# Performance work log

Measured on AMD Instinct MI355X. Metric: run time of the kernel, lower is better.

## Reference

```python
import jax, jax.numpy as jnp
import numpy as np

B, S, NH = 8, 32, 8
N = S * S + 1            # 1 extra (cls) token + S*S image tokens
C = 512
D = C // NH
SCALE = D ** -0.5
LAM = 0.6


def _ln(x, w, b, eps=1e-5):
    m = x.mean(-1, keepdims=True)
    v = ((x - m) ** 2).mean(-1, keepdims=True)
    return (x - m) / jnp.sqrt(v + eps) * w + b


def _rel_index():
    ch, cw = np.meshgrid(np.arange(S), np.arange(S), indexing='ij')
    cf = np.stack([ch.ravel(), cw.ravel()])            # [2, S*S]
    rel = (cf[:, :, None] - cf[:, None, :]).transpose(1, 2, 0).astype(np.int64)
    rel[..., 0] += S - 1
    rel[..., 1] += S - 1
    rel[..., 0] *= 2 * S - 1
    idx = rel.sum(-1)                                  # [n, n]
    out = np.zeros((N, N), dtype=np.int64)             # F.pad with 0 for extra token row/col
    out[1:, 1:] = idx
    return jnp.asarray(out)


def setup_inputs():
    key = jax.random.key(0)
    ks = jax.random.split(key, 8)
    std = 0.02
    return {
        'x': jax.random.normal(ks[0], (B, N, C), jnp.float32),
        'ln1_w': jnp.ones((C,), jnp.float32), 'ln1_b': jnp.zeros((C,), jnp.float32),
        'qkv_w': jax.random.normal(ks[1], (3 * C, C), jnp.float32) * std,
        'rpb_table': jax.random.normal(ks[2], ((2 * S - 1) * (2 * S - 1) + 1, NH), jnp.float32) * std,
        'proj_w': jax.random.normal(ks[3], (C, C), jnp.float32) * std,
        'proj_b': jnp.zeros((C,), jnp.float32),
        'token_weights': jnp.array([0.5, 0.5], jnp.float32),
        'ln2_w': jnp.ones((C,), jnp.float32), 'ln2_b': jnp.zeros((C,), jnp.float32),
        'fc1_w': jax.random.normal(ks[4], (4 * C, C), jnp.float32) * std,
        'fc1_b': jnp.zeros((4 * C,), jnp.float32),
        'fc2_w': jax.random.normal(ks[5], (C, 4 * C), jnp.float32) * std,
        'fc2_b': jnp.zeros((C,), jnp.float32),
        'rel_index': _rel_index(),
        'H': S, 'W': S,
    }


def _attn_core(xn, qkv_w, rpb_table, rel_index):
    qkv = (xn @ qkv_w.T).reshape(B, N, 3, NH, D).transpose(2, 0, 3, 1, 4)
    q, k, v = qkv[0] * SCALE, qkv[1], qkv[2]           # [B, NH, N, D]
    bias = rpb_table[rel_index].transpose(2, 0, 1)     # [NH, N, N] bias-table gather
    attn = jax.nn.softmax(jnp.einsum('bhnd,bhmd->bhnm', q, k) + bias[None], axis=-1)
    out = jnp.einsum('bhnm,bhmd->bhnd', attn, v).transpose(0, 2, 1, 3).reshape(B, N, C)
    return attn, out


def _plan(attn, token_weights):
    # Non-differentiable token-selection plan (pure index computation).
    a = np.asarray(attn)
    cls = a[:, :, 0, 1:].mean(axis=1)                  # [B, n] head-averaged cls->image attn
    n = cls.shape[1]
    avg = cls.mean(1, keepdims=True)
    mx = cls.max(1, keepdims=True)
    counts = ((cls >= avg) & (cls <= mx)).sum(1)
    max_value = int(counts.max())
    T = float(counts.mean())
    sig = 1.0 / (1.0 + np.exp(-(max_value - T) / B))
    keep = int(round(n * (LAM + (1.0 - LAM) * sig)))
    top = np.argsort(-cls, axis=1)[:, :keep].reshape(-1)   # per-batch top-k, flattened
    _, first = np.unique(top, return_index=True)
    sel = top[np.sort(first)][:keep]                   # dedup (first occurrence), truncate
    remaining = N - (1 + keep)
    w = np.asarray(jax.nn.softmax(token_weights))
    nt = int(w[0] * remaining)
    ni = remaining - nt
    kk = jax.random.key(1234)
    ti = jax.random.randint(kk, (B, nt), 0, 1)         # text pool has exactly 1 token
    ii = jax.random.randint(jax.random.fold_in(kk, 1), (B, ni), 0, n - 1)
    return jnp.asarray(sel), ti, ii


def _gather_tok(t, idx):
    return jnp.take_along_axis(t, jnp.broadcast_to(idx[:, :, None], idx.shape + (t.shape[-1],)), axis=1)


def _assemble(xo, xn, sel, ti, ii):
    parts = [xo[:, :1], xo[:, 1:][:, sel],             # kept extra + selected image tokens
             _gather_tok(xn[:, 1:2], ti),              # random 'text' filler from y=xn
             _gather_tok(xn[:, 2:], ii)]               # random 'image' filler from y=xn
    return jnp.concatenate(parts, axis=1)


def reference(x, ln1_w, ln1_b, qkv_w, rpb_table, proj_w, proj_b, token_weights, ln2_w, ln2_b, fc1_w, fc1_b, fc2_w, fc2_b, rel_index, H, W):
    xn = _ln(x, ln1_w, ln1_b)
    attn, out = _attn_core(xn, qkv_w, rpb_table, rel_index)
    xo = out @ proj_w.T + proj_b
    sel, ti, ii = _plan(attn, token_weights)
    x1 = x + _assemble(xo, xn, sel, ti, ii)
    h = _ln(x1, ln2_w, ln2_b)
    h = jax.nn.gelu(h @ fc1_w.T + fc1_b, approximate=False)
    return x1 + (h @ fc2_w.T + fc2_b)
```

## Files before the change

### kernel.cpp

```cpp
#include <hip/hip_runtime.h>
#include <cmath>

#define PARTITIONABLE 1

constexpr int B_ = 8;
constexpr int N_ = 1025;
constexpr int C_ = 512;
constexpr int NH_ = 8;
constexpr int D_ = 64;
constexpr int K3_ = 1536;
constexpr int F_ = 2048;
constexpr int ROWS_ = B_ * N_;
constexpr int NXCD_ = 8;
constexpr int WCONV_BLKS_ = (K3_ * C_ + C_ * C_ + F_ * C_ + C_ * F_) / 1024;

constexpr size_t BYTE_XN      = 0;
constexpr size_t BYTE_QKVBF   = 16793600;
constexpr size_t BYTE_XNBF    = 41984000;
constexpr size_t BYTE_HBUF    = 16793600;
constexpr size_t BYTE_WTAIL   = 60882944;
constexpr size_t BYTE_ATTNBF  = 67174400;
constexpr size_t BYTE_X1NBF   = 75571200;
constexpr size_t BYTE_XO      = 83968000;
constexpr size_t BYTE_X1      = 100761600;
constexpr size_t PLAN_BYTE    = 117555200;

typedef unsigned short u16;
typedef __attribute__((ext_vector_type(4))) unsigned short u16x4;
typedef __attribute__((ext_vector_type(8))) short bf16x8;
typedef __attribute__((ext_vector_type(4))) float f32x4;

__device__ inline u16 f2bf(float f) {
  unsigned u = __float_as_uint(f);
  u = (u + 0x7FFFu + ((u >> 16) & 1u)) >> 16;
  return (u16)u;
}
__device__ inline float bf2f(u16 u) { return __uint_as_float(((unsigned)u) << 16); }

__device__ inline int xcd_swz(int bid, int nwg) {
  const int xcd = bid % NXCD_, i = bid / NXCD_;
  const int q = nwg / NXCD_, r = nwg % NXCD_;
  const int base = (xcd < r) ? xcd * (q + 1) : r * (q + 1) + (xcd - r) * q;
  return base + i;
}

__device__ inline void gload_lds16(const void* g, void* l) {
  __builtin_amdgcn_global_load_lds(
      (const __attribute__((address_space(1))) void*)g,
      (__attribute__((address_space(3))) void*)l, 16, 0, 0);
}

__global__ __launch_bounds__(256) void ln_wconv_kernel(
    const float* __restrict__ x, const float* __restrict__ w,
    const float* __restrict__ b, float* __restrict__ of, u16* __restrict__ ob,
    const float* __restrict__ w0, const float* __restrict__ w1,
    const float* __restrict__ w2, const float* __restrict__ w3,
    u16* __restrict__ o0, u16* __restrict__ o1,
    u16* __restrict__ o2, u16* __restrict__ o3) {
  __shared__ float red[4];
  if (blockIdx.x >= ROWS_) {
    constexpr int n0 = K3_ * C_, n1 = C_ * C_, n2 = F_ * C_;
    const int idx4 = ((blockIdx.x - ROWS_) * 256 + threadIdx.x) * 4;
    const float* src;
    u16* dst;
    int off;
    if (idx4 < n0) { src = w0; dst = o0; off = idx4; }
    else if (idx4 < n0 + n1) { src = w1; dst = o1; off = idx4 - n0; }
    else if (idx4 < n0 + n1 + n2) { src = w2; dst = o2; off = idx4 - n0 - n1; }
    else { src = w3; dst = o3; off = idx4 - n0 - n1 - n2; }
    const float4 v = *(const float4*)(src + off);
    u16x4 r;
    r.x = f2bf(v.x); r.y = f2bf(v.y); r.z = f2bf(v.z); r.w = f2bf(v.w);
    *(u16x4*)(dst + off) = r;
    return;
  }
  const int r = blockIdx.x;
  const int t = threadIdx.x;
  const float* xr = x + (size_t)r * C_;
  float v0 = xr[t], v1 = xr[t + 256];
  float s = v0 + v1;
#pragma unroll
  for (int o = 32; o; o >>= 1) s += __shfl_down(s, o);
  if ((t & 63) == 0) red[t >> 6] = s;
  __syncthreads();
  const float mean = (red[0] + red[1] + red[2] + red[3]) * (1.0f / 512.0f);
  __syncthreads();
  const float d0 = v0 - mean, d1 = v1 - mean;
  float q = d0 * d0 + d1 * d1;
#pragma unroll
  for (int o = 32; o; o >>= 1) q += __shfl_down(q, o);
  if ((t & 63) == 0) red[t >> 6] = q;
  __syncthreads();
  const float var = (red[0] + red[1] + red[2] + red[3]) * (1.0f / 512.0f);
  const float inv = 1.0f / sqrtf(var + 1e-5f);
  const float r0 = d0 * inv * w[t] + b[t];
  const float r1 = d1 * inv * w[t + 256] + b[t + 256];
  of[(size_t)r * C_ + t] = r0;
  of[(size_t)r * C_ + t + 256] = r1;
  ob[(size_t)r * C_ + t] = f2bf(r0);
  ob[(size_t)r * C_ + t + 256] = f2bf(r1);
}

template <int BN, int ACT, bool RES, bool OUTBF, bool QSCALE>
__global__ __launch_bounds__(256) void gemm_bf_kernel(
    const u16* __restrict__ A, const u16* __restrict__ W,
    const float* __restrict__ bias, const float* __restrict__ resid,
    void* __restrict__ outp, int M, int K, int Nout) {
  constexpr int WN = BN / 2;
  constexpr int NJ = WN / 16;
  constexpr int BPW = (BN / 8) / 4;
  __shared__ alignas(16) u16 As[2][128][64];
  __shared__ alignas(16) u16 Bs[2][BN][64];
  const int tid = threadIdx.x;
  const int ny = Nout / BN;
  const int l = xcd_swz(blockIdx.x, gridDim.x);
  const int m0 = (l / ny) * 128, n0 = (l % ny) * BN;
  const int wave = tid >> 6, lane = tid & 63;
  const int wr = wave >> 1, wc = wave & 1;
  const int lrow = lane & 15, lgrp = lane >> 4;
  const int srow = lane >> 3;
  const int soff = (16 * (lane & 7)) ^ (16 * srow);
  const int nk = K >> 6;

  auto stage = [&](int k0, int bufi) {
#pragma unroll
    for (int c = 0; c < 4; ++c) {
      const int q = wave * 4 + c;
      const int row = q * 8 + srow;
      int gm = m0 + row;
      if (gm >= M) gm = M - 1;
      gload_lds16((const char*)(A + (size_t)gm * K + k0) + soff,
                  (char*)&As[bufi][0][0] + (q << 10));
    }
#pragma unroll
    for (int c = 0; c < BPW; ++c) {
      const int q = wave * BPW + c;
      const int row = q * 8 + srow;
      gload_lds16((const char*)(W + (size_t)(n0 + row) * K + k0) + soff,
                  (char*)&Bs[bufi][0][0] + (q << 10));
    }
  };

  f32x4 acc[4][NJ] = {};
  stage(0, 0);
  int buf = 0;
  for (int t = 0; t < nk; ++t) {
    if (t + 1 < nk) {
      stage((t + 1) << 6, buf ^ 1);
      if constexpr (BN == 128) asm volatile("s_waitcnt vmcnt(8)" ::: "memory");
      else                     asm volatile("s_waitcnt vmcnt(6)" ::: "memory");
    } else {
      asm volatile("s_waitcnt vmcnt(0)" ::: "memory");
    }
    __builtin_amdgcn_sched_barrier(0);
    __builtin_amdgcn_s_barrier();
    const char* asb = (const char*)&As[buf][0][0];
    const char* bsb = (const char*)&Bs[buf][0][0];
    __builtin_amdgcn_s_setprio(1);
#pragma unroll
    for (int ch = 0; ch < 2; ++ch) {
      bf16x8 af[4], bfv[NJ];
#pragma unroll
      for (int i = 0; i < 4; ++i) {
        const int ra = wr * 64 + i * 16 + lrow;
        const int cb = ch * 64 + lgrp * 16;
        af[i] = *(const bf16x8*)(asb + (ra << 7) + (cb ^ ((ra & 7) << 4)));
      }
#pragma unroll
      for (int j = 0; j < NJ; ++j) {
        const int rb = wc * WN + j * 16 + lrow;
        const int cb = ch * 64 + lgrp * 16;
        bfv[j] = *(const bf16x8*)(bsb + (rb << 7) + (cb ^ ((rb & 7) << 4)));
      }
#pragma unroll
      for (int i = 0; i < 4; ++i)
#pragma unroll
        for (int j = 0; j < NJ; ++j)
          acc[i][j] = __builtin_amdgcn_mfma_f32_16x16x32_bf16(af[i], bfv[j], acc[i][j], 0, 0, 0);
    }
    __builtin_amdgcn_s_setprio(0);
    asm volatile("s_waitcnt lgkmcnt(0)" ::: "memory");
    __builtin_amdgcn_sched_barrier(0);
    __builtin_amdgcn_s_barrier();
    buf ^= 1;
  }
#pragma unroll
  for (int i = 0; i < 4; ++i) {
#pragma unroll
    for (int j = 0; j < NJ; ++j) {
#pragma unroll
      for (int reg = 0; reg < 4; ++reg) {
        const int gm = m0 + wr * 64 + i * 16 + lgrp * 4 + reg;
        if (gm >= M) continue;
        const int gn = n0 + wc * WN + j * 16 + lrow;
        float v = acc[i][j][reg];
        if (bias) v += bias[gn];
        if (ACT == 1) v = 0.5f * v * (1.0f + erff(v * 0.70710678118654752440f));
        if (QSCALE) { if (gn < 512) v *= 0.125f; }
        if (RES) v += resid[(size_t)gm * Nout + gn];
        if (OUTBF) ((u16*)outp)[(size_t)gm * Nout + gn] = f2bf(v);
        else       ((float*)outp)[(size_t)gm * Nout + gn] = v;
      }
    }
  }
}

__global__ __launch_bounds__(256) void pack_kv_kernel(const u16* __restrict__ qkvbf,
                                                      u16* __restrict__ kb,
                                                      u16* __restrict__ vb) {
  const int tile = blockIdx.x, h = blockIdx.y, b = blockIdx.z;
  const int t = threadIdx.x;
  __shared__ u16 Vt[64][72];
  const int krow = tile * 64 + (t >> 2);
  const int dseg = (t & 3) * 16;
  const u16* p = qkvbf + (size_t)(b * N_ + krow) * K3_ + 512 + h * D_ + dseg;
  const bf16x8 k0 = *(const bf16x8*)p;
  const bf16x8 k1 = *(const bf16x8*)(p + 8);
  u16* kp = kb + ((size_t)(b * NH_ + h) * 1024 + krow) * 64 + dseg;
  *(bf16x8*)kp = k0;
  *(bf16x8*)(kp + 8) = k1;
  const bf16x8 v0 = *(const bf16x8*)(p + 512);
  const bf16x8 v1 = *(const bf16x8*)(p + 520);
  *(bf16x8*)(&Vt[t >> 2][dseg]) = v0;
  *(bf16x8*)(&Vt[t >> 2][dseg + 8]) = v1;
  __syncthreads();
  const int d = t >> 2, kseg = (t & 3) * 16;
  bf16x8 o0, o1;
#pragma unroll
  for (int i = 0; i < 8; ++i) o0[i] = (short)Vt[kseg + i][d];
#pragma unroll
  for (int i = 0; i < 8; ++i) o1[i] = (short)Vt[kseg + 8 + i][d];
  u16* vp = vb + ((size_t)(b * NH_ + h) * 64 + d) * 1024 + tile * 64 + kseg;
  *(bf16x8*)vp = o0;
  *(bf16x8*)(vp + 8) = o1;
}

__global__ __launch_bounds__(256) void attn_mfma_kernel(
    const u16* __restrict__ qkvbf, const u16* __restrict__ kb,
    const u16* __restrict__ vb, const float* __restrict__ rpb,
    u16* __restrict__ attnout) {
  const int l = xcd_swz(blockIdx.x, gridDim.x);
  const int qt = l % 17;
  const int bh = l / 17;
  const int h = bh & 7, b = bh >> 3;
  const int wave = threadIdx.x >> 6, lane = threadIdx.x & 63;
  const int lrow = lane & 15, lgrp = lane >> 4;
  const int qblk = qt * 64;
  const int qbase = qblk + wave * 16;
  __shared__ alignas(16) u16 Ks[2][64][64];
  __shared__ alignas(16) u16 Vs[2][64][64];
  __shared__ alignas(16) u16 Pl[4][16][74];
  __shared__ float tab[35 * 63];

  const u16* kpan = kb + (size_t)(b * NH_ + h) * 1024 * 64;
  const u16* vpan = vb + (size_t)(b * NH_ + h) * 64 * 1024;

#pragma unroll
  for (int c = 0; c < 2; ++c) {
    const int Y = ((wave * 2 + c) << 10) | (lane << 4);
    const int Ys = Y ^ (((Y >> 7) & 7) << 4);
    gload_lds16((const char*)kpan + Ys, (char*)&Ks[0][0][0] + ((wave * 2 + c) << 10));
    const int row = Y >> 7;
    gload_lds16((const char*)vpan + (size_t)row * 2048 + (Ys & 127),
                (char*)&Vs[0][0][0] + ((wave * 2 + c) << 10));
  }

  const int qimin = max(qblk - 1, 0);
  const int qimax = min(qblk + 62, 1023);
  const int qymin = qimin >> 5;
  const int qymax = qimax >> 5;
  const int nrows = qymax - qymin + 32;
  for (int i = threadIdx.x; i < nrows * 63; i += 256)
    tab[i] = rpb[(size_t)(qymin * 63 + i) * NH_ + h];

  u16 (*pl)[74] = Pl[wave];

  bf16x8 qf[2];
  {
    const int qrow = min(qbase + lrow, N_ - 1);
    const u16* qp = qkvbf + (size_t)(b * N_ + qrow) * K3_ + h * D_;
    qf[0] = *(const bf16x8*)(qp + lgrp * 8);
    qf[1] = *(const bf16x8*)(qp + 32 + lgrp * 8);
  }

  const float bias0 = rpb[h];

  int AlocR[4];
  bool qclsR[4];
#pragma unroll
  for (int reg = 0; reg < 4; ++reg) {
    const int qr = min(qbase + lgrp * 4 + reg, N_ - 1);
    const int qi = max(qr - 1, 0);
    AlocR[reg] = ((qi >> 5) - qymin + 31) * 63 + (qi & 31) + 31;
    qclsR[reg] = (qr == 0);
  }

  f32x4 psum = {0.f, 0.f, 0.f, 0.f};
  f32x4 o[4] = {};

  __syncthreads();

  for (int t = 0; t < 16; ++t) {
    const int buf = t & 1;
    if (t < 15) {
      const int keybase = (t + 1) * 64;
#pragma unroll
      for (int c = 0; c < 2; ++c) {
        const int Y = ((wave * 2 + c) << 10) | (lane << 4);
        const int Ys = Y ^ (((Y >> 7) & 7) << 4);
        gload_lds16((const char*)kpan + ((size_t)keybase << 7) + Ys,
                    (char*)&Ks[buf ^ 1][0][0] + ((wave * 2 + c) << 10));
        const int row = Y >> 7;
        gload_lds16((const char*)vpan + (size_t)row * 2048 + ((size_t)keybase << 1) + (Ys & 127),
                    (char*)&Vs[buf ^ 1][0][0] + ((wave * 2 + c) << 10));
      }
      asm volatile("s_waitcnt vmcnt(4)" ::: "memory");
    } else {
      asm volatile("s_waitcnt vmcnt(0)" ::: "memory");
    }
    __builtin_amdgcn_sched_barrier(0);
    __builtin_amdgcn_s_barrier();

    const int keybase = t * 64;
    const char* ksb = (const char*)&Ks[buf][0][0];
    const char* vsb = (const char*)&Vs[buf][0][0];

    f32x4 s[4] = {};
    __builtin_amdgcn_s_setprio(1);
#pragma unroll
    for (int tile = 0; tile < 4; ++tile) {
      const int row = tile * 16 + lrow;
      const int sw = (row & 7) << 4;
      const bf16x8 kf0 = *(const bf16x8*)(ksb + ((row * 128 + lgrp * 16) ^ sw));
      const bf16x8 kf1 = *(const bf16x8*)(ksb + ((row * 128 + 64 + lgrp * 16) ^ sw));
      s[tile] = __builtin_amdgcn_mfma_f32_16x16x32_bf16(qf[0], kf0, s[tile], 0, 0, 0);
      s[tile] = __builtin_amdgcn_mfma_f32_16x16x32_bf16(qf[1], kf1, s[tile], 0, 0, 0);
    }
    __builtin_amdgcn_s_setprio(0);
#pragma unroll
    for (int tile = 0; tile < 4; ++tile) {
      const int key = keybase + tile * 16 + lrow;
      const int ki = max(key - 1, 0);
      const int kpart = (ki >> 5) * 63 + (ki & 31);
      const bool kcls = (key == 0);
#pragma unroll
      for (int reg = 0; reg < 4; ++reg) {
        const float bias = (qclsR[reg] || kcls) ? bias0 : tab[AlocR[reg] - kpart];
        const float p = __expf(s[tile][reg] + bias);
        psum[reg] += p;
        pl[lgrp * 4 + reg][tile * 16 + lrow] = f2bf(p);
      }
    }
    __builtin_amdgcn_s_setprio(1);
#pragma unroll
    for (int ch = 0; ch < 2; ++ch) {
      const bf16x8 pf = *(const bf16x8*)(&pl[lrow][ch * 32 + lgrp * 8]);
#pragma unroll
      for (int dt = 0; dt < 4; ++dt) {
        const int row = dt * 16 + lrow;
        const bf16x8 vf = *(const bf16x8*)(vsb + ((row * 128 + ch * 64 + lgrp * 16) ^ ((row & 7) << 4)));
        o[dt] = __builtin_amdgcn_mfma_f32_16x16x32_bf16(pf, vf, o[dt], 0, 0, 0);
      }
    }
    __builtin_amdgcn_s_setprio(0);
    asm volatile("s_waitcnt lgkmcnt(0)" ::: "memory");
    __builtin_amdgcn_sched_barrier(0);
    __builtin_amdgcn_s_barrier();
  }

#pragma unroll
  for (int reg = 0; reg < 4; ++reg) {
    float v = psum[reg];
    v += __shfl_xor(v, 1);
    v += __shfl_xor(v, 2);
    v += __shfl_xor(v, 4);
    v += __shfl_xor(v, 8);
    psum[reg] = v;
  }

  float ptail;
  {
    const u16* k1p = qkvbf + (size_t)(b * N_ + 1024) * K3_ + 512 + h * D_;
    const bf16x8 k10 = *(const bf16x8*)(k1p + lgrp * 8);
    const bf16x8 k11 = *(const bf16x8*)(k1p + 32 + lgrp * 8);
    float part = 0.f;
#pragma unroll
    for (int i = 0; i < 8; ++i)
      part += bf2f((u16)qf[0][i]) * bf2f((u16)k10[i]) + bf2f((u16)qf[1][i]) * bf2f((u16)k11[i]);
    part += __shfl_xor(part, 16);
    part += __shfl_xor(part, 32);
    const int q_s = min(qbase + lrow, N_ - 1);
    const int qi_s = max(q_s - 1, 0);
    const int Aloc_s = ((qi_s >> 5) - qymin + 31) * 63 + (qi_s & 31) + 31;
    const float btail = (q_s == 0) ? bias0 : tab[Aloc_s - 31 * 63 - 31];
    ptail = __expf(part + btail);
  }

  float v1024[4];
#pragma unroll
  for (int dt = 0; dt < 4; ++dt)
    v1024[dt] = bf2f(qkvbf[(size_t)(b * N_ + 1024) * K3_ + 1024 + h * D_ + dt * 16 + lrow]);

#pragma unroll
  for (int reg = 0; reg < 4; ++reg) {
    const float pr = __shfl(ptail, lgrp * 4 + reg);
    const int qrow = qbase + lgrp * 4 + reg;
    if (qrow >= N_) continue;
    const float inv = 1.0f / (psum[reg] + pr);
    u16* op = attnout + (size_t)(b * N_ + qrow) * C_ + h * D_ + lrow;
#pragma unroll
    for (int dt = 0; dt < 4; ++dt)
      op[dt * 16] = f2bf((o[dt][reg] + pr * v1024[dt]) * inv);
  }
}

__global__ __launch_bounds__(256) void plan_q0_kernel(const float* __restrict__ xn,
                                                      const float* __restrict__ qkvw,
                                                      double* __restrict__ q0) {
  const int idx = blockIdx.x * 256 + threadIdx.x;
  const int b = idx >> 9, hd = idx & 511;
  const float* xr = xn + (size_t)(b * N_) * C_;
  const float* wr = qkvw + (size_t)hd * C_;
  double s = 0.0;
  for (int c = 0; c < C_; c += 4) {
    const float4 xv = *(const float4*)(xr + c);
    const float4 wv = *(const float4*)(wr + c);
    s += (double)xv.x * (double)wv.x;
    s += (double)xv.y * (double)wv.y;
    s += (double)xv.z * (double)wv.z;
    s += (double)xv.w * (double)wv.w;
  }
  q0[idx] = s * 0.125;
}

__global__ __launch_bounds__(256) void plan_u_kernel(const float* __restrict__ qkvw,
                                                     const double* __restrict__ q0,
                                                     double* __restrict__ u) {
  const int idx = blockIdx.x * 256 + threadIdx.x;
  const int b = idx >> 12, h = (idx >> 9) & 7, c = idx & 511;
  double s = 0.0;
  for (int d = 0; d < D_; ++d)
    s += q0[b * 512 + h * 64 + d] * (double)qkvw[(size_t)(512 + h * 64 + d) * C_ + c];
  u[idx] = s;
}

__global__ __launch_bounds__(256) void plan_logit_kernel(const float* __restrict__ xn,
                                                         const double* __restrict__ u,
                                                         double* __restrict__ lgt) {
  __shared__ double ul[8][512];
  const int b = blockIdx.y;
  const int m = blockIdx.x * 256 + threadIdx.x;
  for (int i = threadIdx.x; i < 4096; i += 256)
    ((double*)ul)[i] = u[(size_t)b * 4096 + i];
  __syncthreads();
  if (m >= N_) return;
  const float* xr = xn + (size_t)(b * N_ + m) * C_;
  double s[8] = {};
  for (int c = 0; c < C_; c += 4) {
    const float4 xv = *(const float4*)(xr + c);
#pragma unroll
    for (int hh = 0; hh < 8; ++hh) {
      s[hh] += (double)xv.x * ul[hh][c];
      s[hh] += (double)xv.y * ul[hh][c + 1];
      s[hh] += (double)xv.z * ul[hh][c + 2];
      s[hh] += (double)xv.w * ul[hh][c + 3];
    }
  }
#pragma unroll
  for (int hh = 0; hh < 8; ++hh)
    lgt[(size_t)(b * 8 + hh) * N_ + m] = s[hh];
}

__global__ __launch_bounds__(256) void plan_softmax_kernel(const double* __restrict__ lgt,
                                                           double* __restrict__ mxz) {
  __shared__ double red[4];
  const int bh = blockIdx.x, t = threadIdx.x;
  const double* row = lgt + (size_t)bh * N_;
  double m = -1e300;
  for (int i = t; i < N_; i += 256) m = fmax(m, row[i]);
#pragma unroll
  for (int o = 32; o; o >>= 1) m = fmax(m, __shfl_down(m, o));
  if ((t & 63) == 0) red[t >> 6] = m;
  __syncthreads();
  const double mx = fmax(fmax(red[0], red[1]), fmax(red[2], red[3]));
  __syncthreads();
  double z = 0.0;
  for (int i = t; i < N_; i += 256) z += exp(row[i] - mx);
#pragma unroll
  for (int o = 32; o; o >>= 1) z += __shfl_down(z, o);
  if ((t & 63) == 0) red[t >> 6] = z;
  __syncthreads();
  if (t == 0) {
    mxz[bh] = mx;
    mxz[64 + bh] = red[0] + red[1] + red[2] + red[3];
  }
}

__global__ __launch_bounds__(256) void plan_cls_kernel(const double* __restrict__ lgt,
                                                       const double* __restrict__ mxz,
                                                       double* __restrict__ cls) {
  const int idx = blockIdx.x * 256 + threadIdx.x;
  const int b = idx >> 10, i = idx & 1023;
  double s = 0.0;
  for (int h = 0; h < 8; ++h) {
    const int bh = b * 8 + h;
    s += exp(lgt[(size_t)bh * N_ + 1 + i] - mxz[bh]) / mxz[64 + bh];
  }
  cls[idx] = s / 8.0;
}

__device__ inline void tf2x32(unsigned k0, unsigned k1, unsigned& x0, unsigned& x1) {
  const unsigned ks2 = k0 ^ k1 ^ 0x1BD11BDAu;
  const int r0[4] = {13, 15, 26, 6};
  const int r1[4] = {17, 29, 16, 24};
  x0 += k0; x1 += k1;
#pragma unroll
  for (int i = 0; i < 4; ++i) { x0 += x1; x1 = (x1 << r0[i]) | (x1 >> (32 - r0[i])); x1 ^= x0; }
  x0 += k1; x1 += ks2 + 1u;
#pragma unroll
  for (int i = 0; i < 4; ++i) { x0 += x1; x1 = (x1 << r1[i]) | (x1 >> (32 - r1[i])); x1 ^= x0; }
  x0 += ks2; x1 += k0 + 2u;
#pragma unroll
  for (int i = 0; i < 4; ++i) { x0 += x1; x1 = (x1 << r0[i]) | (x1 >> (32 - r0[i])); x1 ^= x0; }
  x0 += k0; x1 += k1 + 3u;
#pragma unroll
  for (int i = 0; i < 4; ++i) { x0 += x1; x1 = (x1 << r1[i]) | (x1 >> (32 - r1[i])); x1 ^= x0; }
  x0 += k1; x1 += ks2 + 4u;
#pragma unroll
  for (int i = 0; i < 4; ++i) { x0 += x1; x1 = (x1 << r0[i]) | (x1 >> (32 - r0[i])); x1 ^= x0; }
  x0 += ks2; x1 += k0 + 5u;
}

__global__ __launch_bounds__(1024) void plan_tail_kernel(
    const double* __restrict__ cls, const float* __restrict__ tw,
    int* __restrict__ scal, int* __restrict__ sel, int* __restrict__ ii) {
  __shared__ double sv[1024];
  __shared__ int sid[1024];
  __shared__ double dred[16];
  __shared__ int ired[16];
  __shared__ double stats[2];
  __shared__ int cnts[8];
  __shared__ int sc3[3];
  const int t = threadIdx.x;
  const int wid = t >> 6, lane = t & 63;

  sv[t] = cls[t];
  sid[t] = t;
  __syncthreads();
  for (int k = 2; k <= 1024; k <<= 1) {
    for (int j = k >> 1; j > 0; j >>= 1) {
      const int ixj = t ^ j;
      if (ixj > t) {
        const double va = sv[t], vb = sv[ixj];
        const int ia = sid[t], ib = sid[ixj];
        const bool aFirst = (va > vb) || (va == vb && ia < ib);
        const bool desc = ((t & k) == 0);
        if (desc ? (!aFirst) : aFirst) {
          sv[t] = vb; sv[ixj] = va;
          sid[t] = ib; sid[ixj] = ia;
        }
      }
      __syncthreads();
    }
  }
  sel[t] = sid[t];
  __syncthreads();

  for (int b = 0; b < 8; ++b) {
    const double val = cls[b * 1024 + t];
    double s = val;
#pragma unroll
    for (int o = 32; o; o >>= 1) s += __shfl_down(s, o);
    if (lane == 0) dred[wid] = s;
    __syncthreads();
    if (t == 0) {
      double tot = 0;
      for (int i = 0; i < 16; ++i) tot += dred[i];
      stats[0] = tot / 1024.0;
    }
    __syncthreads();
    double mv = val;
#pragma unroll
    for (int o = 32; o; o >>= 1) mv = fmax(mv, __shfl_down(mv, o));
    if (lane == 0) dred[wid] = mv;
    __syncthreads();
    if (t == 0) {
      double mx = dred[0];
      for (int i = 1; i < 16; ++i) mx = fmax(mx, dred[i]);
      stats[1] = mx;
    }
    __syncthreads();
    int c = (val >= stats[0] && val <= stats[1]) ? 1 : 0;
#pragma unroll
    for (int o = 32; o; o >>= 1) c += __shfl_down(c, o);
    if (lane == 0) ired[wid] = c;
    __syncthreads();
    if (t == 0) {
      int cc = 0;
      for (int i = 0; i < 16; ++i) cc += ired[i];
      cnts[b] = cc;
    }
    __syncthreads();
  }

  if (t == 0) {
    int maxv = 0;
    double sum = 0.0;
    for (int b = 0; b < 8; ++b) {
      maxv = max(maxv, cnts[b]);
      sum += (double)cnts[b];
    }
    const double T = sum / 8.0;
    const double sig = 1.0 / (1.0 + exp(-((double)maxv - T) / 8.0));
    const double keepf = 1024.0 * (0.6 + (1.0 - 0.6) * sig);
    const int keep = __double2int_rn(keepf);
    const int remaining = 1024 - keep;
    const float t0 = tw[0], t1 = tw[1];
    const float mw = fmaxf(t0, t1);
    const float e0 = expf(t0 - mw), e1 = expf(t1 - mw);
    const float w0 = e0 / (e0 + e1);
    const int nt = (int)(w0 * (float)remaining);
    const int ni = remaining - nt;
    scal[0] = keep; scal[1] = nt; scal[2] = ni;
    sc3[0] = keep; sc3[1] = nt; sc3[2] = ni;
  }
  __syncthreads();

  const int ni = sc3[2];
  const int size = 8 * ni;
  const unsigned span = 1023u;
  unsigned mult = 65536u % span;
  mult = (mult * mult) % span;
  unsigned f0 = 0u, f1 = 1u;
  tf2x32(0u, 1234u, f0, f1);
#if PARTITIONABLE
  unsigned k1a = 0u, k1b = 0u;
  tf2x32(f0, f1, k1a, k1b);
  unsigned k2a = 0u, k2b = 1u;
  tf2x32(f0, f1, k2a, k2b);
  for (int i = t; i < size; i += 1024) {
    unsigned h0 = 0u, h1 = (unsigned)i;
    tf2x32(k1a, k1b, h0, h1);
    const unsigned hb = h0 ^ h1;
    unsigned l0 = 0u, l1 = (unsigned)i;
    tf2x32(k2a, k2b, l0, l1);
    const unsigned lb = l0 ^ l1;
    ii[i] = (int)(((hb % span) * mult + (lb % span)) % span);
  }
#else
  unsigned a0 = 0u, a1 = 2u;
  tf2x32(f0, f1, a0, a1);
  unsigned b0 = 1u, b1 = 3u;
  tf2x32(f0, f1, b0, b1);
  const int half = size >> 1;
  for (int i = t; i < half; i += 1024) {
    unsigned h0 = (unsigned)i, h1 = (unsigned)(i + half);
    tf2x32(a0, b0, h0, h1);
    unsigned l0 = (unsigned)i, l1 = (unsigned)(i + half);
    tf2x32(a1, b1, l0, l1);
    ii[i]        = (int)(((h0 % span) * mult + (l0 % span)) % span);
    ii[i + half] = (int)(((h1 % span) * mult + (l1 % span)) % span);
  }
#endif
}

__global__ __launch_bounds__(256) void assemble_ln_kernel(
    const float* __restrict__ x, const float* __restrict__ xn,
    const float* __restrict__ xo, const int* __restrict__ scal,
    const int* __restrict__ sel, const int* __restrict__ ii,
    const float* __restrict__ w, const float* __restrict__ bb,
    float* __restrict__ x1, u16* __restrict__ ob) {
  __shared__ float red[4];
  const int blk = blockIdx.x;
  const int b = blk / N_, tok = blk % N_;
  const int keep = scal[0], nt = scal[1], ni = scal[2];
  const float* src;
  if (tok == 0) {
    src = xo + (size_t)(b * N_) * C_;
  } else if (tok <= keep) {
    src = xo + (size_t)(b * N_ + 1 + sel[tok - 1]) * C_;
  } else if (tok <= keep + nt) {
    src = xn + (size_t)(b * N_ + 1) * C_;
  } else {
    const int j = tok - 1 - keep - nt;
    src = xn + (size_t)(b * N_ + 2 + ii[b * ni + j]) * C_;
  }
  const int t = threadIdx.x;
  const size_t o = (size_t)blk * C_;
  const float v0 = x[o + t] + src[t];
  const float v1 = x[o + t + 256] + src[t + 256];
  x1[o + t] = v0;
  x1[o + t + 256] = v1;
  float s = v0 + v1;
#pragma unroll
  for (int of = 32; of; of >>= 1) s += __shfl_down(s, of);
  if ((t & 63) == 0) red[t >> 6] = s;
  __syncthreads();
  const float mean = (red[0] + red[1] + red[2] + red[3]) * (1.0f / 512.0f);
  __syncthreads();
  const float d0 = v0 - mean, d1 = v1 - mean;
  float q = d0 * d0 + d1 * d1;
#pragma unroll
  for (int of = 32; of; of >>= 1) q += __shfl_down(q, of);
  if ((t & 63) == 0) red[t >> 6] = q;
  __syncthreads();
  const float var = (red[0] + red[1] + red[2] + red[3]) * (1.0f / 512.0f);
  const float inv = 1.0f / sqrtf(var + 1e-5f);
  ob[o + t] = f2bf(d0 * inv * w[t] + bb[t]);
  ob[o + t + 256] = f2bf(d1 * inv * w[t + 256] + bb[t + 256]);
}

extern "C" void kernel_launch(void* const* d_in, const int* in_sizes, int n_in,
                              void* d_out, int out_size, void* d_ws, size_t ws_size,
                              hipStream_t stream) {
  (void)in_sizes; (void)n_in; (void)out_size; (void)ws_size;
  const float* x     = (const float*)d_in[0];
  const float* ln1w  = (const float*)d_in[1];
  const float* ln1b  = (const float*)d_in[2];
  const float* qkvw  = (const float*)d_in[3];
  const float* rpb   = (const float*)d_in[4];
  const float* projw = (const float*)d_in[5];
  const float* projb = (const float*)d_in[6];
  const float* tw    = (const float*)d_in[7];
  const float* ln2w  = (const float*)d_in[8];
  const float* ln2b  = (const float*)d_in[9];
  const float* fc1w  = (const float*)d_in[10];
  const float* fc1b  = (const float*)d_in[11];
  const float* fc2w  = (const float*)d_in[12];
  const float* fc2b  = (const float*)d_in[13];
  float* out = (float*)d_out;
  char* base = (char*)d_ws;

  float* xn       = (float*)(base + BYTE_XN);
  u16*   qkv_bf   = (u16*)(base + BYTE_QKVBF);
  u16*   xn_bf    = (u16*)(base + BYTE_XNBF);
  u16*   hbuf     = (u16*)(base + BYTE_HBUF);
  u16*   wq_bf    = (u16*)(base + BYTE_WTAIL);
  u16*   wp_bf    = wq_bf + K3_ * C_;
  u16*   w1_bf    = wp_bf + C_ * C_;
  u16*   w2_bf    = w1_bf + F_ * C_;
  u16*   attn_bf  = (u16*)(base + BYTE_ATTNBF);
  u16*   x1n_bf   = (u16*)(base + BYTE_X1NBF);
  float* xo       = (float*)(base + BYTE_XO);
  u16*   kbuf     = (u16*)(base + BYTE_X1);
  u16*   vbuf     = kbuf + (size_t)B_ * NH_ * 1024 * 64;
  float* x1       = (float*)(base + BYTE_X1);

  char* pb = base + PLAN_BYTE;
  double* q0  = (double*)pb;
  double* u   = q0 + 4096;
  double* lgt = u + 32768;
  double* mxz = lgt + 65600;
  double* cls = mxz + 128;
  int* counts = (int*)(cls + 8192);
  int* scal   = counts + 8;
  int* sel    = scal + 4;
  int* iibuf  = sel + 1024;

  ln_wconv_kernel<<<ROWS_ + WCONV_BLKS_, 256, 0, stream>>>(
      x, ln1w, ln1b, xn, xn_bf,
      qkvw, projw, fc1w, fc2w, wq_bf, wp_bf, w1_bf, w2_bf);
  gemm_bf_kernel<128, 0, false, true, true><<<65 * 12, 256, 0, stream>>>(
      xn_bf, wq_bf, nullptr, nullptr, qkv_bf, ROWS_, C_, K3_);
  pack_kv_kernel<<<dim3(16, NH_, B_), 256, 0, stream>>>(qkv_bf, kbuf, vbuf);
  plan_q0_kernel<<<16, 256, 0, stream>>>(xn, qkvw, q0);
  plan_u_kernel<<<128, 256, 0, stream>>>(qkvw, q0, u);
  plan_logit_kernel<<<dim3(5, B_), 256, 0, stream>>>(xn, u, lgt);
  plan_softmax_kernel<<<64, 256, 0, stream>>>(lgt, mxz);
  plan_cls_kernel<<<32, 256, 0, stream>>>(lgt, mxz, cls);
  plan_tail_kernel<<<1, 1024, 0, stream>>>(cls, tw, scal, sel, iibuf);
  attn_mfma_kernel<<<17 * NH_ * B_, 256, 0, stream>>>(
      qkv_bf, kbuf, vbuf, rpb, attn_bf);
  gemm_bf_kernel<64, 0, false, false, false><<<65 * 8, 256, 0, stream>>>(
      attn_bf, wp_bf, projb, nullptr, xo, ROWS_, C_, C_);
  assemble_ln_kernel<<<ROWS_, 256, 0, stream>>>(
      x, xn, xo, scal, sel, iibuf, ln2w, ln2b, x1, x1n_bf);
  gemm_bf_kernel<128, 1, false, true, false><<<65 * 16, 256, 0, stream>>>(
      x1n_bf, w1_bf, fc1b, nullptr, hbuf, ROWS_, C_, F_);
  gemm_bf_kernel<64, 0, true, false, false><<<65 * 8, 256, 0, stream>>>(
      hbuf, w2_bf, fc2b, x1, out, ROWS_, F_, C_);
}
```

Before: 371.8 us.

## Enlarge attention query tile to 96 rows with 6 waves and split K/V loading

The attention kernel now uses 384 threads (6 waves) per block, each block covering 96 query rows instead of 64. This cuts the grid from 17 to 11 tiles per head and reuses each K/V tile across more queries, reducing global K/V traffic. K loads are now issued by waves 0-3 and V loads by waves 4-5, with per-wave waitcnt values. The relative-position bias table in LDS is stored as bf16 to offset the larger Pl buffer, which loses some bias precision; the larger block may also lower occupancy.

After: 370.8 us (median of 2 runs). No clear change (-0.3%).

```diff
diff --git a/kernel.cpp b/kernel.cpp
--- a/kernel.cpp
+++ b/kernel.cpp
@@ -235,43 +235,53 @@
   *(bf16x8*)(vp + 8) = o1;
 }
 
-__global__ __launch_bounds__(256) void attn_mfma_kernel(
+__global__ __launch_bounds__(384) void attn_mfma_kernel(
     const u16* __restrict__ qkvbf, const u16* __restrict__ kb,
     const u16* __restrict__ vb, const float* __restrict__ rpb,
     u16* __restrict__ attnout) {
   const int l = xcd_swz(blockIdx.x, gridDim.x);
-  const int qt = l % 17;
-  const int bh = l / 17;
+  const int qt = l % 11;
+  const int bh = l / 11;
   const int h = bh & 7, b = bh >> 3;
   const int wave = threadIdx.x >> 6, lane = threadIdx.x & 63;
   const int lrow = lane & 15, lgrp = lane >> 4;
-  const int qblk = qt * 64;
+  const int qblk = qt * 96;
   const int qbase = qblk + wave * 16;
   __shared__ alignas(16) u16 Ks[2][64][64];
   __shared__ alignas(16) u16 Vs[2][64][64];
-  __shared__ alignas(16) u16 Pl[4][16][74];
-  __shared__ float tab[35 * 63];
+  __shared__ alignas(16) u16 Pl[6][16][74];
+  __shared__ u16 tab[36 * 63];
 
   const u16* kpan = kb + (size_t)(b * NH_ + h) * 1024 * 64;
   const u16* vpan = vb + (size_t)(b * NH_ + h) * 64 * 1024;
 
-#pragma unroll
-  for (int c = 0; c < 2; ++c) {
-    const int Y = ((wave * 2 + c) << 10) | (lane << 4);
-    const int Ys = Y ^ (((Y >> 7) & 7) << 4);
-    gload_lds16((const char*)kpan + Ys, (char*)&Ks[0][0][0] + ((wave * 2 + c) << 10));
-    const int row = Y >> 7;
-    gload_lds16((const char*)vpan + (size_t)row * 2048 + (Ys & 127),
-                (char*)&Vs[0][0][0] + ((wave * 2 + c) << 10));
+  if (wave < 4) {
+#pragma unroll
+    for (int c = 0; c < 2; ++c) {
+      const int q = wave * 2 + c;
+      const int Y = (q << 10) | (lane << 4);
+      const int Ys = Y ^ (((Y >> 7) & 7) << 4);
+      gload_lds16((const char*)kpan + Ys, (char*)&Ks[0][0][0] + (q << 10));
+    }
+  } else {
+#pragma unroll
+    for (int c = 0; c < 4; ++c) {
+      const int q = (wave - 4) * 4 + c;
+      const int Y = (q << 10) | (lane << 4);
+      const int Ys = Y ^ (((Y >> 7) & 7) << 4);
+      const int row = Y >> 7;
+      gload_lds16((const char*)vpan + (size_t)row * 2048 + (Ys & 127),
+                  (char*)&Vs[0][0][0] + (q << 10));
+    }
   }
 
   const int qimin = max(qblk - 1, 0);
-  const int qimax = min(qblk + 62, 1023);
+  const int qimax = min(qblk + 94, 1023);
   const int qymin = qimin >> 5;
   const int qymax = qimax >> 5;
   const int nrows = qymax - qymin + 32;
-  for (int i = threadIdx.x; i < nrows * 63; i += 256)
-    tab[i] = rpb[(size_t)(qymin * 63 + i) * NH_ + h];
+  for (int i = threadIdx.x; i < nrows * 63; i += 384)
+    tab[i] = f2bf(rpb[(size_t)(qymin * 63 + i) * NH_ + h]);
 
   u16 (*pl)[74] = Pl[wave];
 
@@ -303,18 +313,29 @@
   for (int t = 0; t < 16; ++t) {
     const int buf = t & 1;
     if (t < 15) {
-      const int keybase = (t + 1) * 64;
-#pragma unroll
-      for (int c = 0; c < 2; ++c) {
-        const int Y = ((wave * 2 + c) << 10) | (lane << 4);
-        const int Ys = Y ^ (((Y >> 7) & 7) << 4);
-        gload_lds16((const char*)kpan + ((size_t)keybase << 7) + Ys,
-                    (char*)&Ks[buf ^ 1][0][0] + ((wave * 2 + c) << 10));
-        const int row = Y >> 7;
-        gload_lds16((const char*)vpan + (size_t)row * 2048 + ((size_t)keybase << 1) + (Ys & 127),
-                    (char*)&Vs[buf ^ 1][0][0] + ((wave * 2 + c) << 10));
+      const int keybase2 = (t + 1) * 64;
+      if (wave < 4) {
+#pragma unroll
+        for (int c = 0; c < 2; ++c) {
+          const int q = wave * 2 + c;
+          const int Y = (q << 10) | (lane << 4);
+          const int Ys = Y ^ (((Y >> 7) & 7) << 4);
+          gload_lds16((const char*)kpan + ((size_t)keybase2 << 7) + Ys,
+                      (char*)&Ks[buf ^ 1][0][0] + (q << 10));
+        }
+        asm volatile("s_waitcnt vmcnt(2)" ::: "memory");
+      } else {
+#pragma unroll
+        for (int c = 0; c < 4; ++c) {
+          const int q = (wave - 4) * 4 + c;
+          const int Y = (q << 10) | (lane << 4);
+          const int Ys = Y ^ (((Y >> 7) & 7) << 4);
+          const int row = Y >> 7;
+          gload_lds16((const char*)vpan + (size_t)row * 2048 + ((size_t)keybase2 << 1) + (Ys & 127),
+                      (char*)&Vs[buf ^ 1][0][0] + (q << 10));
+        }
+        asm volatile("s_waitcnt vmcnt(4)" ::: "memory");
       }
-      asm volatile("s_waitcnt vmcnt(4)" ::: "memory");
     } else {
       asm volatile("s_waitcnt vmcnt(0)" ::: "memory");
     }
@@ -345,7 +366,7 @@
       const bool kcls = (key == 0);
 #pragma unroll
       for (int reg = 0; reg < 4; ++reg) {
-        const float bias = (qclsR[reg] || kcls) ? bias0 : tab[AlocR[reg] - kpart];
+        const float bias = (qclsR[reg] || kcls) ? bias0 : bf2f(tab[AlocR[reg] - kpart]);
         const float p = __expf(s[tile][reg] + bias);
         psum[reg] += p;
         pl[lgrp * 4 + reg][tile * 16 + lrow] = f2bf(p);
@@ -392,7 +413,7 @@
     const int q_s = min(qbase + lrow, N_ - 1);
     const int qi_s = max(q_s - 1, 0);
     const int Aloc_s = ((qi_s >> 5) - qymin + 31) * 63 + (qi_s & 31) + 31;
-    const float btail = (q_s == 0) ? bias0 : tab[Aloc_s - 31 * 63 - 31];
+    const float btail = (q_s == 0) ? bias0 : bf2f(tab[Aloc_s - 31 * 63 - 31]);
     ptail = __expf(part + btail);
   }
 
@@ -769,7 +790,7 @@
   plan_softmax_kernel<<<64, 256, 0, stream>>>(lgt, mxz);
   plan_cls_kernel<<<32, 256, 0, stream>>>(lgt, mxz, cls);
   plan_tail_kernel<<<1, 1024, 0, stream>>>(cls, tw, scal, sel, iibuf);
-  attn_mfma_kernel<<<17 * NH_ * B_, 256, 0, stream>>>(
+  attn_mfma_kernel<<<11 * NH_ * B_, 384, 0, stream>>>(
       qkv_bf, kbuf, vbuf, rpb, attn_bf);
   gemm_bf_kernel<64, 0, false, false, false><<<65 * 8, 256, 0, stream>>>(
       attn_bf, wp_bf, projb, nullptr, xo, ROWS_, C_, C_);
```
